# Optimization experiments

Measured on AMD Instinct MI355X. Metric: run time of the kernel, lower is better.

The kernel has to match this reference:

```python
import jax, jax.numpy as jnp
import numpy as np

N_NODES = 100000
N_EDGES = 1600000
DIM = 64
N_LAYERS = 6


def setup_inputs() -> dict:
    key = jax.random.key(0)
    ks = jax.random.split(key, 4)
    x = jax.random.normal(ks[0], (N_NODES, DIM), dtype=jnp.float32)
    edge_index = jax.random.randint(ks[1], (2, N_EDGES), 0, N_NODES, dtype=jnp.int64)
    # SAGEConv params per layer: lin_l (neighbor, with bias), lin_r (root, no bias)
    Wl = jax.random.normal(ks[2], (N_LAYERS, DIM, DIM), dtype=jnp.float32) * 0.05
    bl = jnp.zeros((N_LAYERS, DIM), dtype=jnp.float32)
    Wr = jax.random.normal(ks[3], (N_LAYERS, DIM, DIM), dtype=jnp.float32) * 0.05
    return {"x": x, "edge_index": edge_index, "Wl": Wl, "bl": bl, "Wr": Wr}


def reference(x, edge_index, Wl, bl, Wr):
    src, dst = edge_index[0], edge_index[1]
    n = x.shape[0]

    def sage(h, W_l, b_l, W_r):
        # gather neighbor features [E, D], scatter-max into dst nodes [N, D]
        agg = jax.ops.segment_max(h[src], dst, num_segments=n)
        # nodes with no in-edges get -inf from segment_max -> 0 (PyG convention)
        agg = jnp.where(jnp.isneginf(agg), jnp.zeros((), h.dtype), agg)
        return agg @ W_l.T + b_l + h @ W_r.T

    h = x
    for i in range(N_LAYERS):
        h = sage(h, Wl[i], bl[i], Wr[i])
        if i < N_LAYERS - 1:
            h = jax.nn.relu(h)
        # dropout (p=0.1) is identity in eval mode
    return h
```

## Files before the change

kernel.cpp:

```cpp
#include <hip/hip_runtime.h>
#include <hip/hip_bf16.h>
#include <math.h>

#define DIM 64

typedef _Float16 half_t;
typedef __attribute__((ext_vector_type(8))) _Float16 half8;
typedef __attribute__((ext_vector_type(4))) _Float16 h16x4;
typedef __attribute__((ext_vector_type(4))) float f32x4;

__device__ __forceinline__ half8 hmax8(half8 a, half8 b) {
    return __builtin_elementwise_max(a, b);
}


__global__ void kbcnt(const int* __restrict__ ei, int E, int* __restrict__ gcnt) {
    __shared__ int h[256];
    int t = threadIdx.x;
    h[t] = 0;
    __syncthreads();
    for (int e = blockIdx.x * 256 + t; e < E; e += gridDim.x * 256)
        atomicAdd(&h[ei[E + e] >> 9], 1);
    __syncthreads();
    if (h[t]) atomicAdd(&gcnt[t], h[t]);
}

__global__ void kbscan(const int* __restrict__ gcnt, int* __restrict__ gbs,
                       int* __restrict__ gbc, int NB, int E,
                       int* __restrict__ rs, int N) {
    __shared__ int sm[256];
    int t = threadIdx.x;
    int v = (t < NB) ? gcnt[t] : 0;
    sm[t] = v;
    __syncthreads();
    for (int off = 1; off < 256; off <<= 1) {
        int add = (t >= off) ? sm[t - off] : 0;
        __syncthreads();
        sm[t] += add;
        __syncthreads();
    }
    int excl = sm[t] - v;
    if (t < NB) { gbs[t] = excl; gbc[t] = excl; }
    if (t == NB - 1) gbs[NB] = excl + v;
    if (t == 0) rs[N] = E;
}

__global__ void kbin(const int* __restrict__ ei, int E,
                     int* __restrict__ gbc, int* __restrict__ pairs, int NB) {
    __shared__ int hist[256];
    __shared__ int basep[256];
    const int t = threadIdx.x;
    const int c0 = blockIdx.x * 4096;
    hist[t] = 0;
    __syncthreads();
    int s[16], d[16];
#pragma unroll
    for (int i = 0; i < 16; ++i) {
        int e = c0 + i * 256 + t;
        if (e < E) {
            s[i] = ei[e];
            d[i] = ei[E + e];
            atomicAdd(&hist[d[i] >> 9], 1);
        } else d[i] = -1;
    }
    __syncthreads();
    if (t < NB) {
        basep[t] = atomicAdd(&gbc[t], hist[t]);
        hist[t] = 0;
    }
    __syncthreads();
#pragma unroll
    for (int i = 0; i < 16; ++i) {
        if (d[i] >= 0) {
            int b = d[i] >> 9;
            int off = atomicAdd(&hist[b], 1);
            pairs[basep[b] + off] = (s[i] << 9) | (d[i] & 511);
        }
    }
}

__global__ void __launch_bounds__(256) kfinal(
        const int* __restrict__ pairs, const int* __restrict__ gbs,
        int* __restrict__ rs, int* __restrict__ ssrc, int N) {
    __shared__ int lcnt[512];
    __shared__ int lcur[512];
    __shared__ int ps[256];
    const int b = blockIdx.x;
    const int t = threadIdx.x;
    const int n0 = b << 9;
    const int e0 = gbs[b], e1 = gbs[b + 1];
    lcnt[t] = 0;
    lcnt[t + 256] = 0;
    __syncthreads();
    for (int e = e0 + t; e < e1; e += 256)
        atomicAdd(&lcnt[pairs[e] & 511], 1);
    __syncthreads();
    int c0 = lcnt[2 * t], c1 = lcnt[2 * t + 1];
    int sum = c0 + c1;
    ps[t] = sum;
    __syncthreads();
    for (int off = 1; off < 256; off <<= 1) {
        int add = (t >= off) ? ps[t - off] : 0;
        __syncthreads();
        ps[t] += add;
        __syncthreads();
    }
    int excl = ps[t] - sum;
    lcur[2 * t] = excl;
    lcur[2 * t + 1] = excl + c0;
    int n = n0 + 2 * t;
    if (n < N) rs[n] = e0 + excl;
    if (n + 1 < N) rs[n + 1] = e0 + excl + c0;
    __syncthreads();
    for (int e = e0 + t; e < e1; e += 256) {
        int p = pairs[e];
        int pos = atomicAdd(&lcur[p & 511], 1);
        ssrc[e0 + pos] = (int)((unsigned)p >> 9) << 7;
    }
}


__global__ void kcvt(const float* __restrict__ x, half_t* __restrict__ phi, int n4) {
    int i = blockIdx.x * blockDim.x + threadIdx.x;
    if (i < n4) {
        f32x4 v = ((const f32x4*)x)[i];
        h16x4 hi;
#pragma unroll
        for (int c = 0; c < 4; ++c) hi[c] = (half_t)v[c];
        ((h16x4*)phi)[i] = hi;
    }
}


__global__ void kprepw(const float* __restrict__ Wl, const float* __restrict__ Wr,
                       half_t* __restrict__ Bf) {
    int id = blockIdx.x * blockDim.x + threadIdx.x;
    if (id >= 6 * 4 * 4 * 64 * 8) return;
    int i = id & 7;
    int lane = (id >> 3) & 63;
    int t = (id >> 9) & 3;
    int s = (id >> 11) & 3;
    int layer = id >> 13;
    int k = s * 32 + (lane >> 4) * 8 + i;
    int j = t * 16 + (lane & 15);
    float v = (k < 64) ? Wl[(layer * 64 + j) * 64 + k]
                       : Wr[(layer * 64 + j) * 64 + (k - 64)];
    half_t hi = (half_t)v;
    half_t lo = (half_t)(v - (float)hi);
    int f = (s * 4 + t) * 2;
    int base = layer * 16384 + f * 512 + lane * 8 + i;
    Bf[base] = hi;
    Bf[base + 512] = lo;
}


__global__ void __launch_bounds__(256, 2) kfused(
        const half_t* __restrict__ hin, const int* __restrict__ rs,
        const int* __restrict__ soff, const half_t* __restrict__ Bf,
        const float* __restrict__ bias, float* __restrict__ out32,
        half_t* __restrict__ hout, int N, int last) {
    const int lane = threadIdx.x & 63;
    const int quad = lane >> 4;
    const int lrow = lane & 15;
    const int wv = (blockIdx.x * blockDim.x + threadIdx.x) >> 6;
    const int nwv = (gridDim.x * blockDim.x) >> 6;
    const int ntiles = (N + 15) >> 4;

    const half8* __restrict__ Bp = (const half8*)Bf;
    half8 bh[4][4], bl[4][4];
#pragma unroll
    for (int s = 0; s < 4; ++s)
#pragma unroll
        for (int t = 0; t < 4; ++t) {
            int f = (s * 4 + t) * 2;
            bh[s][t] = Bp[f * 64 + lane];
            bl[s][t] = Bp[f * 64 + 64 + lane];
        }

    float bs[4];
#pragma unroll
    for (int t = 0; t < 4; ++t) bs[t] = bias[t * 16 + lrow];

    const char* hq = (const char*)hin + quad * 16;
    const half_t NEG = (half_t)(-65504.0f);

    for (int tile = wv; tile < ntiles; tile += nwv) {
        const int m0 = tile << 4;
        int row = m0 + lrow;
        if (row >= N) row = N - 1;

        const char* ph = (const char*)hin + (size_t)row * 128 + quad * 16;
        half8 Hh0 = *(const half8*)(ph);
        half8 Hh1 = *(const half8*)(ph + 64);

        int beg = rs[row], end = rs[row + 1];
        int lastE = end - 1;
        half8 m0a = {NEG, NEG, NEG, NEG, NEG, NEG, NEG, NEG};
        half8 m1a = m0a, m2a = m0a, m3a = m0a;
        half8 m0b = m0a, m1b = m0a, m2b = m0a, m3b = m0a;
        for (int e = beg; e < end; e += 4) {
            int e1 = (e + 1 <= lastE) ? e + 1 : lastE;
            int e2 = (e + 2 <= lastE) ? e + 2 : lastE;
            int e3 = (e + 3 <= lastE) ? e + 3 : lastE;
            int o0 = soff[e], o1 = soff[e1], o2 = soff[e2], o3 = soff[e3];
            m0a = hmax8(m0a, *(const half8*)(hq + o0));
            m0b = hmax8(m0b, *(const half8*)(hq + o0 + 64));
            m1a = hmax8(m1a, *(const half8*)(hq + o1));
            m1b = hmax8(m1b, *(const half8*)(hq + o1 + 64));
            m2a = hmax8(m2a, *(const half8*)(hq + o2));
            m2b = hmax8(m2b, *(const half8*)(hq + o2 + 64));
            m3a = hmax8(m3a, *(const half8*)(hq + o3));
            m3b = hmax8(m3b, *(const half8*)(hq + o3 + 64));
        }
        half8 Aa0 = hmax8(hmax8(m0a, m1a), hmax8(m2a, m3a));
        half8 Aa1 = hmax8(hmax8(m0b, m1b), hmax8(m2b, m3b));
        if (end <= beg) {
            half8 z = {(half_t)0.f, (half_t)0.f, (half_t)0.f, (half_t)0.f,
                       (half_t)0.f, (half_t)0.f, (half_t)0.f, (half_t)0.f};
            Aa0 = z; Aa1 = z;
        }

        f32x4 acc[4] = {{0.f, 0.f, 0.f, 0.f}, {0.f, 0.f, 0.f, 0.f},
                        {0.f, 0.f, 0.f, 0.f}, {0.f, 0.f, 0.f, 0.f}};
#pragma unroll
        for (int t = 0; t < 4; ++t) {
            acc[t] = __builtin_amdgcn_mfma_f32_16x16x32_f16(Aa0, bh[0][t], acc[t], 0, 0, 0);
            acc[t] = __builtin_amdgcn_mfma_f32_16x16x32_f16(Aa0, bl[0][t], acc[t], 0, 0, 0);
            acc[t] = __builtin_amdgcn_mfma_f32_16x16x32_f16(Aa1, bh[1][t], acc[t], 0, 0, 0);
            acc[t] = __builtin_amdgcn_mfma_f32_16x16x32_f16(Aa1, bl[1][t], acc[t], 0, 0, 0);
            acc[t] = __builtin_amdgcn_mfma_f32_16x16x32_f16(Hh0, bh[2][t], acc[t], 0, 0, 0);
            acc[t] = __builtin_amdgcn_mfma_f32_16x16x32_f16(Hh0, bl[2][t], acc[t], 0, 0, 0);
            acc[t] = __builtin_amdgcn_mfma_f32_16x16x32_f16(Hh1, bh[3][t], acc[t], 0, 0, 0);
            acc[t] = __builtin_amdgcn_mfma_f32_16x16x32_f16(Hh1, bl[3][t], acc[t], 0, 0, 0);
        }

#pragma unroll
        for (int t = 0; t < 4; ++t) {
            int col = t * 16 + lrow;
#pragma unroll
            for (int r = 0; r < 4; ++r) {
                int orow = m0 + quad * 4 + r;
                if (orow < N) {
                    float v = acc[t][r] + bs[t];
                    if (!last) {
                        v = fmaxf(v, 0.0f);
                        hout[(size_t)orow * DIM + col] = (half_t)v;
                    } else {
                        out32[(size_t)orow * DIM + col] = v;
                    }
                }
            }
        }
    }
}


extern "C" void kernel_launch(void* const* d_in, const int* in_sizes, int n_in,
                              void* d_out, int out_size, void* d_ws, size_t ws_size,
                              hipStream_t stream) {
    const float* x  = (const float*)d_in[0];
    const int*   ei = (const int*)d_in[1];
    const float* Wl = (const float*)d_in[2];
    const float* bl = (const float*)d_in[3];
    const float* Wr = (const float*)d_in[4];
    int N = in_sizes[0] / DIM;
    int E = in_sizes[1] / 2;

    size_t nd = (size_t)N * DIM;
    half_t* p0    = (half_t*)d_ws;
    half_t* p1    = p0 + nd;
    half_t* scratch = p1 + nd;
    int*    rs    = (int*)(scratch + nd);
    int*    ssrc  = rs + (N + 4);
    int*    gcnt  = ssrc + E;
    int*    gbs   = gcnt + 256;
    int*    gbc   = gbs + 260;
    half_t* Bf    = (half_t*)(gbc + 256);

    int NB = (N + 511) >> 9;
    int* pairs = (int*)scratch;

    hipMemsetAsync(gcnt, 0, 256 * sizeof(int), stream);
    kbcnt<<<640, 256, 0, stream>>>(ei, E, gcnt);
    kbscan<<<1, 256, 0, stream>>>(gcnt, gbs, gbc, NB, E, rs, N);
    kbin<<<(E + 4095) / 4096, 256, 0, stream>>>(ei, E, gbc, pairs, NB);
    kfinal<<<NB, 256, 0, stream>>>(pairs, gbs, rs, ssrc, N);
    kprepw<<<(6 * 4 * 4 * 64 * 8 + 255) / 256, 256, 0, stream>>>(Wl, Wr, Bf);
    kcvt<<<((int)(nd / 4) + 255) / 256, 256, 0, stream>>>(x, p0, (int)(nd / 4));

    for (int l = 0; l < 6; ++l) {
        half_t* ih = (l & 1) ? p1 : p0;
        half_t* oh = (l & 1) ? p0 : p1;
        int last = (l == 5);
        kfused<<<512, 256, 0, stream>>>(ih, rs, ssrc, Bf + l * 16384, bl + l * 64,
                                        (float*)d_out, oh, N, last);
    }
}
```

Baseline: 442.1 us.

## Stage weight fragments in LDS and launch one tile per wave

The split-fp16 weight fragments move from 32 half8 registers per lane into a 32 KB shared-memory buffer that each block fills cooperatively. This frees VGPRs, so launch bounds rise from 2 to 4 blocks per CU. The grid changes from a fixed 512 blocks with a grid-stride loop to one 16-row tile per wave, which means about 1563 blocks. In exchange, every MFMA now reads its B operand from LDS, and each block must reload the 32 KB of weights, which is repeated for many more blocks.

```diff
diff --git a/kernel.cpp b/kernel.cpp
--- a/kernel.cpp
+++ b/kernel.cpp
@@ -154,28 +154,29 @@
 }
 
 
-__global__ void __launch_bounds__(256, 2) kfused(
+__global__ void __launch_bounds__(256, 4) kfused(
         const half_t* __restrict__ hin, const int* __restrict__ rs,
         const int* __restrict__ soff, const half_t* __restrict__ Bf,
         const float* __restrict__ bias, float* __restrict__ out32,
         half_t* __restrict__ hout, int N, int last) {
-    const int lane = threadIdx.x & 63;
+    __shared__ half_t Bs[16384];
+    const int tid = threadIdx.x;
+    const int lane = tid & 63;
     const int quad = lane >> 4;
     const int lrow = lane & 15;
-    const int wv = (blockIdx.x * blockDim.x + threadIdx.x) >> 6;
+    const int wv = (blockIdx.x * blockDim.x + tid) >> 6;
     const int nwv = (gridDim.x * blockDim.x) >> 6;
     const int ntiles = (N + 15) >> 4;
 
-    const half8* __restrict__ Bp = (const half8*)Bf;
-    half8 bh[4][4], bl[4][4];
-#pragma unroll
-    for (int s = 0; s < 4; ++s)
-#pragma unroll
-        for (int t = 0; t < 4; ++t) {
-            int f = (s * 4 + t) * 2;
-            bh[s][t] = Bp[f * 64 + lane];
-            bl[s][t] = Bp[f * 64 + 64 + lane];
-        }
+    {
+        const half8* __restrict__ Bg = (const half8*)Bf;
+        half8* Bsh = (half8*)Bs;
+#pragma unroll
+        for (int i = 0; i < 8; ++i)
+            Bsh[i * 256 + tid] = Bg[i * 256 + tid];
+    }
+    __syncthreads();
+    const half8* __restrict__ Bls = (const half8*)Bs;
 
     float bs[4];
 #pragma unroll
@@ -224,14 +225,15 @@
                         {0.f, 0.f, 0.f, 0.f}, {0.f, 0.f, 0.f, 0.f}};
 #pragma unroll
         for (int t = 0; t < 4; ++t) {
-            acc[t] = __builtin_amdgcn_mfma_f32_16x16x32_f16(Aa0, bh[0][t], acc[t], 0, 0, 0);
-            acc[t] = __builtin_amdgcn_mfma_f32_16x16x32_f16(Aa0, bl[0][t], acc[t], 0, 0, 0);
-            acc[t] = __builtin_amdgcn_mfma_f32_16x16x32_f16(Aa1, bh[1][t], acc[t], 0, 0, 0);
-            acc[t] = __builtin_amdgcn_mfma_f32_16x16x32_f16(Aa1, bl[1][t], acc[t], 0, 0, 0);
-            acc[t] = __builtin_amdgcn_mfma_f32_16x16x32_f16(Hh0, bh[2][t], acc[t], 0, 0, 0);
-            acc[t] = __builtin_amdgcn_mfma_f32_16x16x32_f16(Hh0, bl[2][t], acc[t], 0, 0, 0);
-            acc[t] = __builtin_amdgcn_mfma_f32_16x16x32_f16(Hh1, bh[3][t], acc[t], 0, 0, 0);
-            acc[t] = __builtin_amdgcn_mfma_f32_16x16x32_f16(Hh1, bl[3][t], acc[t], 0, 0, 0);
+            int f = t * 2;
+            acc[t] = __builtin_amdgcn_mfma_f32_16x16x32_f16(Aa0, Bls[(f     ) * 64 + lane],      acc[t], 0, 0, 0);
+            acc[t] = __builtin_amdgcn_mfma_f32_16x16x32_f16(Aa0, Bls[(f     ) * 64 + 64 + lane], acc[t], 0, 0, 0);
+            acc[t] = __builtin_amdgcn_mfma_f32_16x16x32_f16(Aa1, Bls[(f +  8) * 64 + lane],      acc[t], 0, 0, 0);
+            acc[t] = __builtin_amdgcn_mfma_f32_16x16x32_f16(Aa1, Bls[(f +  8) * 64 + 64 + lane], acc[t], 0, 0, 0);
+            acc[t] = __builtin_amdgcn_mfma_f32_16x16x32_f16(Hh0, Bls[(f + 16) * 64 + lane],      acc[t], 0, 0, 0);
+            acc[t] = __builtin_amdgcn_mfma_f32_16x16x32_f16(Hh0, Bls[(f + 16) * 64 + 64 + lane], acc[t], 0, 0, 0);
+            acc[t] = __builtin_amdgcn_mfma_f32_16x16x32_f16(Hh1, Bls[(f + 24) * 64 + lane],      acc[t], 0, 0, 0);
+            acc[t] = __builtin_amdgcn_mfma_f32_16x16x32_f16(Hh1, Bls[(f + 24) * 64 + 64 + lane], acc[t], 0, 0, 0);
         }
 
 #pragma unroll
@@ -288,11 +290,13 @@
     kprepw<<<(6 * 4 * 4 * 64 * 8 + 255) / 256, 256, 0, stream>>>(Wl, Wr, Bf);
     kcvt<<<((int)(nd / 4) + 255) / 256, 256, 0, stream>>>(x, p0, (int)(nd / 4));
 
+    int ntiles = (N + 15) >> 4;
+    int gblocks = (ntiles + 3) >> 2;
     for (int l = 0; l < 6; ++l) {
         half_t* ih = (l & 1) ? p1 : p0;
         half_t* oh = (l & 1) ? p0 : p1;
         int last = (l == 5);
-        kfused<<<512, 256, 0, stream>>>(ih, rs, ssrc, Bf + l * 16384, bl + l * 64,
-                                        (float*)d_out, oh, N, last);
-    }
-}
+        kfused<<<gblocks, 256, 0, stream>>>(ih, rs, ssrc, Bf + l * 16384, bl + l * 64,
+                                            (float*)d_out, oh, N, last);
+    }
+}
```

Result: slower. 707.1 us (+60.0%).
